# Performance work log

Measured on AMD Instinct MI355X. Metric: run time of the kernel, lower is better.

The kernel has to match this reference:

```python
import jax, jax.numpy as jnp
import numpy as np

MESSAGE_PASSES = 3
HID = 100        # hidden_node_features == message_size
EDGE_F = 4       # n_edge_features
OUT = 100        # readout output dim


def setup_inputs() -> dict:
    key = jax.random.key(0)
    ks = jax.random.split(key, 8)
    B, N = 32, 128
    nodes = jax.random.normal(ks[0], (B, N, HID), dtype=jnp.float32)
    edges = jax.random.uniform(ks[1], (B, N, N, EDGE_F), dtype=jnp.float32)
    s = 1.0 / np.sqrt(HID)
    Wv = jax.random.normal(ks[2], (HID, HID), dtype=jnp.float32) * s
    Ww = jax.random.normal(ks[3], (HID, HID), dtype=jnp.float32) * s
    We = jax.random.normal(ks[4], (EDGE_F, HID), dtype=jnp.float32) * (1.0 / np.sqrt(EDGE_F))
    Wu = jax.random.normal(ks[5], (2 * HID, HID), dtype=jnp.float32) * (1.0 / np.sqrt(2 * HID))
    Wr = jax.random.normal(ks[6], (2 * HID, OUT), dtype=jnp.float32) * (1.0 / np.sqrt(2 * HID))
    return {"nodes": nodes, "edges": edges, "Wv": Wv, "Ww": Ww, "We": We, "Wu": Wu, "Wr": Wr}


def reference(nodes, edges, Wv, Ww, We, Wu, Wr):
    # adjacency[b,v,w] = sum_e edges[b,v,w,e]; nonzero entries define the edge set
    adjacency = edges.sum(axis=-1)                       # [B,N,N]
    edge_mask = adjacency != 0                           # [B,N,N]
    node_mask = adjacency.sum(axis=-1) != 0              # [B,N]

    # edge feature projection is constant across message passes
    e_proj = jnp.einsum('bvwe,eh->bvwh', edges, We)      # [B,N,N,H]

    hidden = nodes                                       # hidden_node_features == node feat dim
    for _ in range(MESSAGE_PASSES):
        # message_terms for every (b, v, w) edge: relu(h_v Wv + h_w Ww + e_vw We)
        pre = (hidden @ Wv)[:, :, None, :] + (hidden @ Ww)[:, None, :, :] + e_proj
        mterms = jnp.where(edge_mask[..., None], jax.nn.relu(pre), 0.0)
        # (same_batch * same_node) matmul == segment-sum over neighbors w
        messages = mterms.sum(axis=2)                    # [B,N,H]
        # update only nodes that appear in the edge set (degree > 0)
        upd = jnp.tanh(jnp.concatenate([hidden, messages], axis=-1) @ Wu)
        hidden = jnp.where(node_mask[..., None], upd, hidden)

    # readout: masked sum-pool of per-node graph terms
    graph_terms = jax.nn.relu(jnp.concatenate([hidden, nodes], axis=-1) @ Wr)  # [B,N,OUT]
    output = jnp.where(node_mask[..., None], graph_terms, 0.0).sum(axis=1)     # [B,OUT]
    return output
```

## Files before the change

### kernel.cpp

```cpp
#include <hip/hip_runtime.h>
#include <math.h>

#define B_   32
#define N_   128
#define H_   100
#define ROWS (B_ * N_)
#define RH   (ROWS * H_)
#define OUTSZ (B_ * H_)

__global__ __launch_bounds__(256, 6) void k_proj0(const float* __restrict__ nodes,
                                                  const float* __restrict__ Ww,
                                                  float* __restrict__ hw,
                                                  float* __restrict__ out) {
    __shared__ float nod_s[2][H_];
    const int row0 = blockIdx.x * 2;
    const int t = threadIdx.x, r = t >> 7, j = t & 127;
    {
        const int gid = blockIdx.x * 256 + t;
        if (gid < OUTSZ) out[gid] = 0.f;
    }
    {
        const float4* ng = (const float4*)(nodes + (size_t)row0 * H_);
        if (t < 50) ((float4*)nod_s)[t] = ng[t];
    }
    __syncthreads();
    if (j >= H_) return;
    const float4* h4p = (const float4*)nod_s[r];
    float wa = 0.f;
#pragma unroll 5
    for (int k4 = 0; k4 < 25; ++k4) {
        const float4 h4 = h4p[k4];
        const int k = k4 * 4;
        wa = fmaf(h4.x, Ww[(k + 0) * H_ + j], wa);
        wa = fmaf(h4.y, Ww[(k + 1) * H_ + j], wa);
        wa = fmaf(h4.z, Ww[(k + 2) * H_ + j], wa);
        wa = fmaf(h4.w, Ww[(k + 3) * H_ + j], wa);
    }
    hw[(size_t)(row0 + r) * H_ + j] = wa;
}

template <int MODE, int INIT_HV>
__global__ __launch_bounds__(256, 6) void k_pass(const float* __restrict__ edges,
                                                 const float* __restrict__ We,
                                                 const float* __restrict__ Wu,
                                                 const float* __restrict__ Wv,
                                                 const float* __restrict__ Ww,
                                                 const float* __restrict__ Wr,
                                                 const float* __restrict__ nodes,
                                                 float* __restrict__ hv_io,
                                                 const float* __restrict__ hw_in,
                                                 float* __restrict__ hw_out,
                                                 const float* __restrict__ hid_in,
                                                 float* __restrict__ hidden,
                                                 float* __restrict__ out) {
    __shared__ float4 e_s[2][N_];
    __shared__ float  asum_part[4];
    __shared__ unsigned qmask_s[2][4];
    __shared__ float  hid_s[2][H_];
    __shared__ float  msg_s[2][H_];
    __shared__ float  hn_s[2][H_];
    __shared__ float  nod_s[2][H_];
    __shared__ float  red_s[2][H_];

    const int bx = blockIdx.x;
    const int cu = bx & 255, slot = bx >> 8;
    const int b = cu >> 3;
    const int vt = (cu & 7) + slot * 8;
    const int row0 = b * N_ + vt * 2;

    const int t = threadIdx.x, r = t >> 7, j = t & 127;
    const int wv = t >> 6, lane = t & 63;
    const int row = row0 + r;
    const bool act = (j < H_);

    {
        const float4* eg = (const float4*)(edges + (size_t)row0 * N_ * 4);
        const float4 e = eg[t];
        e_s[r][j] = e;
        float s = (e.x + e.y) + (e.z + e.w);
        const unsigned long long bal = __ballot(s != 0.f);
        if (lane == 0) {
            qmask_s[wv >> 1][(wv & 1) * 2]     = (unsigned)bal;
            qmask_s[wv >> 1][(wv & 1) * 2 + 1] = (unsigned)(bal >> 32);
        }
#pragma unroll
        for (int off = 32; off > 0; off >>= 1) s += __shfl_down(s, off);
        if (lane == 0) asum_part[wv] = s;
    }
    {
        const float4* hg = (const float4*)(hid_in + (size_t)row0 * H_);
        if (t < 50) ((float4*)hid_s)[t] = hg[t];
        if (MODE == 2) {
            const float4* ng = (const float4*)(nodes + (size_t)row0 * H_);
            if (t < 50) ((float4*)nod_s)[t] = ng[t];
        }
    }
    __syncthreads();

    const float nm = ((asum_part[2 * r] + asum_part[2 * r + 1]) != 0.f) ? 1.f : 0.f;

    if (act) {
        float hvv;
        if (INIT_HV) {
            const float4* h4p = (const float4*)hid_s[r];
            float va = 0.f;
#pragma unroll 5
            for (int k4 = 0; k4 < 25; ++k4) {
                const float4 h4 = h4p[k4];
                const int k = k4 * 4;
                va = fmaf(h4.x, Wv[(k + 0) * H_ + j], va);
                va = fmaf(h4.y, Wv[(k + 1) * H_ + j], va);
                va = fmaf(h4.z, Wv[(k + 2) * H_ + j], va);
                va = fmaf(h4.w, Wv[(k + 3) * H_ + j], va);
            }
            hvv = va;
        } else {
            hvv = hv_io[(size_t)row * H_ + j];
        }
        const float we0 = We[0 * H_ + j], we1 = We[1 * H_ + j];
        const float we2 = We[2 * H_ + j], we3 = We[3 * H_ + j];
        const float* hwp = hw_in + (size_t)b * N_ * H_ + j;
        float acc = 0.f;
        for (int c = 0; c < 4; ++c) {
            const unsigned mq =
                __builtin_amdgcn_readfirstlane(qmask_s[r][c]);
            const float4* ec = &e_s[r][c * 32];
            const float*  hc = hwp + (size_t)(c * 32) * H_;
#pragma unroll 8
            for (int w8 = 0; w8 < 32; ++w8) {
                const float4 e = ec[w8];
                const float  hww = hc[w8 * H_];
                const float  m = ((mq >> w8) & 1u) ? 1.f : 0.f;
                float p = hvv + hww;
                p = fmaf(e.x, we0, p);
                p = fmaf(e.y, we1, p);
                p = fmaf(e.z, we2, p);
                p = fmaf(e.w, we3, p);
                acc = fmaf(m, fmaxf(p, 0.f), acc);
            }
        }
        msg_s[r][j] = acc;
    }
    __syncthreads();

    if (act) {
        const float4* h4p = (const float4*)hid_s[r];
        const float4* m4p = (const float4*)msg_s[r];
        float u = 0.f;
#pragma unroll 5
        for (int k4 = 0; k4 < 25; ++k4) {
            const float4 h4 = h4p[k4];
            const int k = k4 * 4;
            u = fmaf(h4.x, Wu[(k + 0) * H_ + j], u);
            u = fmaf(h4.y, Wu[(k + 1) * H_ + j], u);
            u = fmaf(h4.z, Wu[(k + 2) * H_ + j], u);
            u = fmaf(h4.w, Wu[(k + 3) * H_ + j], u);
        }
#pragma unroll 5
        for (int k4 = 0; k4 < 25; ++k4) {
            const float4 m4 = m4p[k4];
            const int k = H_ + k4 * 4;
            u = fmaf(m4.x, Wu[(k + 0) * H_ + j], u);
            u = fmaf(m4.y, Wu[(k + 1) * H_ + j], u);
            u = fmaf(m4.z, Wu[(k + 2) * H_ + j], u);
            u = fmaf(m4.w, Wu[(k + 3) * H_ + j], u);
        }
        const float nh = (nm != 0.f) ? tanhf(u) : hid_s[r][j];
        hn_s[r][j] = nh;
        if (MODE == 1) hidden[(size_t)row * H_ + j] = nh;
    }
    __syncthreads();

    if (MODE == 1) {
        if (act) {
            const float4* h4p = (const float4*)hn_s[r];
            float va = 0.f, wa = 0.f;
#pragma unroll 5
            for (int k4 = 0; k4 < 25; ++k4) {
                const float4 h4 = h4p[k4];
                const int k = k4 * 4;
                va = fmaf(h4.x, Wv[(k + 0) * H_ + j], va);
                wa = fmaf(h4.x, Ww[(k + 0) * H_ + j], wa);
                va = fmaf(h4.y, Wv[(k + 1) * H_ + j], va);
                wa = fmaf(h4.y, Ww[(k + 1) * H_ + j], wa);
                va = fmaf(h4.z, Wv[(k + 2) * H_ + j], va);
                wa = fmaf(h4.z, Ww[(k + 2) * H_ + j], wa);
                va = fmaf(h4.w, Wv[(k + 3) * H_ + j], va);
                wa = fmaf(h4.w, Ww[(k + 3) * H_ + j], wa);
            }
            hv_io[(size_t)row * H_ + j] = va;
            hw_out[(size_t)row * H_ + j] = wa;
        }
    } else {
        if (act) {
            const float4* h4p = (const float4*)hn_s[r];
            const float4* n4p = (const float4*)nod_s[r];
            float u = 0.f;
#pragma unroll 5
            for (int k4 = 0; k4 < 25; ++k4) {
                const float4 h4 = h4p[k4];
                const int k = k4 * 4;
                u = fmaf(h4.x, Wr[(k + 0) * H_ + j], u);
                u = fmaf(h4.y, Wr[(k + 1) * H_ + j], u);
                u = fmaf(h4.z, Wr[(k + 2) * H_ + j], u);
                u = fmaf(h4.w, Wr[(k + 3) * H_ + j], u);
            }
#pragma unroll 5
            for (int k4 = 0; k4 < 25; ++k4) {
                const float4 n4 = n4p[k4];
                const int k = H_ + k4 * 4;
                u = fmaf(n4.x, Wr[(k + 0) * H_ + j], u);
                u = fmaf(n4.y, Wr[(k + 1) * H_ + j], u);
                u = fmaf(n4.z, Wr[(k + 2) * H_ + j], u);
                u = fmaf(n4.w, Wr[(k + 3) * H_ + j], u);
            }
            red_s[r][j] = nm * fmaxf(u, 0.f);
        }
        __syncthreads();
        if (t < H_) atomicAdd(out + b * H_ + t, red_s[0][t] + red_s[1][t]);
    }
}

extern "C" void kernel_launch(void* const* d_in, const int* in_sizes, int n_in,
                              void* d_out, int out_size, void* d_ws, size_t ws_size,
                              hipStream_t stream) {
    const float* nodes = (const float*)d_in[0];
    const float* edges = (const float*)d_in[1];
    const float* Wv    = (const float*)d_in[2];
    const float* Ww    = (const float*)d_in[3];
    const float* We    = (const float*)d_in[4];
    const float* Wu    = (const float*)d_in[5];
    const float* Wr    = (const float*)d_in[6];
    float* out = (float*)d_out;

    float* hidden = (float*)d_ws;
    float* hv     = hidden + RH;
    float* hwA    = hv + RH;
    float* hwB    = hwA + RH;

    k_proj0<<<ROWS / 2, 256, 0, stream>>>(nodes, Ww, hwA, out);

    k_pass<1, 1><<<ROWS / 2, 256, 0, stream>>>(edges, We, Wu, Wv, Ww, Wr, nodes,
                                               hv, hwA, hwB, nodes, hidden, out);
    k_pass<1, 0><<<ROWS / 2, 256, 0, stream>>>(edges, We, Wu, Wv, Ww, Wr, nodes,
                                               hv, hwB, hwA, hidden, hidden, out);
    k_pass<2, 0><<<ROWS / 2, 256, 0, stream>>>(edges, We, Wu, Wv, Ww, Wr, nodes,
                                               hv, hwA, hwB, hidden, hidden, out);
}
```

Before: 198.9 us.

## Process four rows per block with two rows per thread to reuse loads

```diff
diff --git a/kernel.cpp b/kernel.cpp
--- a/kernel.cpp
+++ b/kernel.cpp
@@ -53,171 +53,236 @@
                                                  const float* __restrict__ hid_in,
                                                  float* __restrict__ hidden,
                                                  float* __restrict__ out) {
-    __shared__ float4 e_s[2][N_];
-    __shared__ float  asum_part[4];
-    __shared__ unsigned qmask_s[2][4];
-    __shared__ float  hid_s[2][H_];
-    __shared__ float  msg_s[2][H_];
-    __shared__ float  hn_s[2][H_];
-    __shared__ float  nod_s[2][H_];
-    __shared__ float  red_s[2][H_];
+    __shared__ float4 e_s[4][N_];
+    __shared__ float  asum_s[4][2];
+    __shared__ unsigned qmask_s[4][4];
+    __shared__ float  hid_s[4][H_];
+    __shared__ float  msg_s[4][H_];
+    __shared__ float  hn_s[4][H_];
+    __shared__ float  nod_s[4][H_];
+    __shared__ float  red_s[4][H_];
 
     const int bx = blockIdx.x;
     const int cu = bx & 255, slot = bx >> 8;
     const int b = cu >> 3;
     const int vt = (cu & 7) + slot * 8;
-    const int row0 = b * N_ + vt * 2;
-
-    const int t = threadIdx.x, r = t >> 7, j = t & 127;
+    const int row0 = b * N_ + vt * 4;
+
+    const int t = threadIdx.x, rg = t >> 7, j = t & 127;
     const int wv = t >> 6, lane = t & 63;
-    const int row = row0 + r;
+    const int ra = rg * 2, rb = ra + 1;
+    const int rowA = row0 + ra, rowB = row0 + rb;
     const bool act = (j < H_);
 
     {
         const float4* eg = (const float4*)(edges + (size_t)row0 * N_ * 4);
-        const float4 e = eg[t];
-        e_s[r][j] = e;
-        float s = (e.x + e.y) + (e.z + e.w);
-        const unsigned long long bal = __ballot(s != 0.f);
-        if (lane == 0) {
-            qmask_s[wv >> 1][(wv & 1) * 2]     = (unsigned)bal;
-            qmask_s[wv >> 1][(wv & 1) * 2 + 1] = (unsigned)(bal >> 32);
-        }
+        float4* es = &e_s[0][0];
 #pragma unroll
-        for (int off = 32; off > 0; off >>= 1) s += __shfl_down(s, off);
-        if (lane == 0) asum_part[wv] = s;
+        for (int q = 0; q < 2; ++q) {
+            const int idx = q * 256 + t;
+            const float4 e = eg[idx];
+            es[idx] = e;
+            float s = (e.x + e.y) + (e.z + e.w);
+            const unsigned long long bal = __ballot(s != 0.f);
+            const int seg = q * 4 + wv;
+            const int rowq = seg >> 1, half = seg & 1;
+            if (lane == 0) {
+                qmask_s[rowq][half * 2]     = (unsigned)bal;
+                qmask_s[rowq][half * 2 + 1] = (unsigned)(bal >> 32);
+            }
+#pragma unroll
+            for (int off = 32; off > 0; off >>= 1) s += __shfl_down(s, off);
+            if (lane == 0) asum_s[rowq][half] = s;
+        }
     }
     {
         const float4* hg = (const float4*)(hid_in + (size_t)row0 * H_);
-        if (t < 50) ((float4*)hid_s)[t] = hg[t];
+        if (t < 100) ((float4*)hid_s)[t] = hg[t];
         if (MODE == 2) {
             const float4* ng = (const float4*)(nodes + (size_t)row0 * H_);
-            if (t < 50) ((float4*)nod_s)[t] = ng[t];
+            if (t < 100) ((float4*)nod_s)[t] = ng[t];
         }
     }
     __syncthreads();
 
-    const float nm = ((asum_part[2 * r] + asum_part[2 * r + 1]) != 0.f) ? 1.f : 0.f;
+    const float nmA = ((asum_s[ra][0] + asum_s[ra][1]) != 0.f) ? 1.f : 0.f;
+    const float nmB = ((asum_s[rb][0] + asum_s[rb][1]) != 0.f) ? 1.f : 0.f;
 
     if (act) {
-        float hvv;
+        float hvA, hvB;
         if (INIT_HV) {
-            const float4* h4p = (const float4*)hid_s[r];
-            float va = 0.f;
+            const float4* hA = (const float4*)hid_s[ra];
+            const float4* hB = (const float4*)hid_s[rb];
+            float vA = 0.f, vB = 0.f;
 #pragma unroll 5
             for (int k4 = 0; k4 < 25; ++k4) {
-                const float4 h4 = h4p[k4];
                 const int k = k4 * 4;
-                va = fmaf(h4.x, Wv[(k + 0) * H_ + j], va);
-                va = fmaf(h4.y, Wv[(k + 1) * H_ + j], va);
-                va = fmaf(h4.z, Wv[(k + 2) * H_ + j], va);
-                va = fmaf(h4.w, Wv[(k + 3) * H_ + j], va);
-            }
-            hvv = va;
+                const float w0 = Wv[(k + 0) * H_ + j];
+                const float w1 = Wv[(k + 1) * H_ + j];
+                const float w2 = Wv[(k + 2) * H_ + j];
+                const float w3 = Wv[(k + 3) * H_ + j];
+                const float4 a = hA[k4], c = hB[k4];
+                vA = fmaf(a.x, w0, vA); vB = fmaf(c.x, w0, vB);
+                vA = fmaf(a.y, w1, vA); vB = fmaf(c.y, w1, vB);
+                vA = fmaf(a.z, w2, vA); vB = fmaf(c.z, w2, vB);
+                vA = fmaf(a.w, w3, vA); vB = fmaf(c.w, w3, vB);
+            }
+            hvA = vA; hvB = vB;
         } else {
-            hvv = hv_io[(size_t)row * H_ + j];
+            hvA = hv_io[(size_t)rowA * H_ + j];
+            hvB = hv_io[(size_t)rowB * H_ + j];
         }
         const float we0 = We[0 * H_ + j], we1 = We[1 * H_ + j];
         const float we2 = We[2 * H_ + j], we3 = We[3 * H_ + j];
         const float* hwp = hw_in + (size_t)b * N_ * H_ + j;
-        float acc = 0.f;
+        float accA = 0.f, accB = 0.f;
         for (int c = 0; c < 4; ++c) {
-            const unsigned mq =
-                __builtin_amdgcn_readfirstlane(qmask_s[r][c]);
-            const float4* ec = &e_s[r][c * 32];
-            const float*  hc = hwp + (size_t)(c * 32) * H_;
+            const unsigned mqA =
+                __builtin_amdgcn_readfirstlane(qmask_s[ra][c]);
+            const unsigned mqB =
+                __builtin_amdgcn_readfirstlane(qmask_s[rb][c]);
+            const float4* ecA = &e_s[ra][c * 32];
+            const float4* ecB = &e_s[rb][c * 32];
+            const float*  hc  = hwp + (size_t)(c * 32) * H_;
 #pragma unroll 8
             for (int w8 = 0; w8 < 32; ++w8) {
-                const float4 e = ec[w8];
-                const float  hww = hc[w8 * H_];
-                const float  m = ((mq >> w8) & 1u) ? 1.f : 0.f;
-                float p = hvv + hww;
-                p = fmaf(e.x, we0, p);
-                p = fmaf(e.y, we1, p);
-                p = fmaf(e.z, we2, p);
-                p = fmaf(e.w, we3, p);
-                acc = fmaf(m, fmaxf(p, 0.f), acc);
-            }
-        }
-        msg_s[r][j] = acc;
+                const float hww = hc[w8 * H_];
+                const float4 eA = ecA[w8];
+                const float4 eB = ecB[w8];
+                float pA = hvA + hww;
+                pA = fmaf(eA.x, we0, pA);
+                pA = fmaf(eA.y, we1, pA);
+                pA = fmaf(eA.z, we2, pA);
+                pA = fmaf(eA.w, we3, pA);
+                const float mA = ((mqA >> w8) & 1u) ? 1.f : 0.f;
+                accA = fmaf(mA, fmaxf(pA, 0.f), accA);
+                float pB = hvB + hww;
+                pB = fmaf(eB.x, we0, pB);
+                pB = fmaf(eB.y, we1, pB);
+                pB = fmaf(eB.z, we2, pB);
+                pB = fmaf(eB.w, we3, pB);
+                const float mB = ((mqB >> w8) & 1u) ? 1.f : 0.f;
+                accB = fmaf(mB, fmaxf(pB, 0.f), accB);
+            }
+        }
+        msg_s[ra][j] = accA;
+        msg_s[rb][j] = accB;
     }
     __syncthreads();
 
+    float nhA, nhB;
     if (act) {
-        const float4* h4p = (const float4*)hid_s[r];
-        const float4* m4p = (const float4*)msg_s[r];
-        float u = 0.f;
+        const float4* hA = (const float4*)hid_s[ra];
+        const float4* hB = (const float4*)hid_s[rb];
+        const float4* mA4 = (const float4*)msg_s[ra];
+        const float4* mB4 = (const float4*)msg_s[rb];
+        float uA = 0.f, uB = 0.f;
 #pragma unroll 5
         for (int k4 = 0; k4 < 25; ++k4) {
-            const float4 h4 = h4p[k4];
             const int k = k4 * 4;
-            u = fmaf(h4.x, Wu[(k + 0) * H_ + j], u);
-            u = fmaf(h4.y, Wu[(k + 1) * H_ + j], u);
-            u = fmaf(h4.z, Wu[(k + 2) * H_ + j], u);
-            u = fmaf(h4.w, Wu[(k + 3) * H_ + j], u);
+            const float w0 = Wu[(k + 0) * H_ + j];
+            const float w1 = Wu[(k + 1) * H_ + j];
+            const float w2 = Wu[(k + 2) * H_ + j];
+            const float w3 = Wu[(k + 3) * H_ + j];
+            const float4 a = hA[k4], c = hB[k4];
+            uA = fmaf(a.x, w0, uA); uB = fmaf(c.x, w0, uB);
+            uA = fmaf(a.y, w1, uA); uB = fmaf(c.y, w1, uB);
+            uA = fmaf(a.z, w2, uA); uB = fmaf(c.z, w2, uB);
+            uA = fmaf(a.w, w3, uA); uB = fmaf(c.w, w3, uB);
         }
 #pragma unroll 5
         for (int k4 = 0; k4 < 25; ++k4) {
-            const float4 m4 = m4p[k4];
             const int k = H_ + k4 * 4;
-            u = fmaf(m4.x, Wu[(k + 0) * H_ + j], u);
-            u = fmaf(m4.y, Wu[(k + 1) * H_ + j], u);
-            u = fmaf(m4.z, Wu[(k + 2) * H_ + j], u);
-            u = fmaf(m4.w, Wu[(k + 3) * H_ + j], u);
-        }
-        const float nh = (nm != 0.f) ? tanhf(u) : hid_s[r][j];
-        hn_s[r][j] = nh;
-        if (MODE == 1) hidden[(size_t)row * H_ + j] = nh;
+            const float w0 = Wu[(k + 0) * H_ + j];
+            const float w1 = Wu[(k + 1) * H_ + j];
+            const float w2 = Wu[(k + 2) * H_ + j];
+            const float w3 = Wu[(k + 3) * H_ + j];
+            const float4 a = mA4[k4], c = mB4[k4];
+            uA = fmaf(a.x, w0, uA); uB = fmaf(c.x, w0, uB);
+            uA = fmaf(a.y, w1, uA); uB = fmaf(c.y, w1, uB);
+            uA = fmaf(a.z, w2, uA); uB = fmaf(c.z, w2, uB);
+            uA = fmaf(a.w, w3, uA); uB = fmaf(c.w, w3, uB);
+        }
+        nhA = (nmA != 0.f) ? tanhf(uA) : hid_s[ra][j];
+        nhB = (nmB != 0.f) ? tanhf(uB) : hid_s[rb][j];
+        hn_s[ra][j] = nhA;
+        hn_s[rb][j] = nhB;
+        if (MODE == 1) {
+            hidden[(size_t)rowA * H_ + j] = nhA;
+            hidden[(size_t)rowB * H_ + j] = nhB;
+        }
     }
     __syncthreads();
 
     if (MODE == 1) {
         if (act) {
-            const float4* h4p = (const float4*)hn_s[r];
-            float va = 0.f, wa = 0.f;
+            const float4* hA = (const float4*)hn_s[ra];
+            const float4* hB = (const float4*)hn_s[rb];
+            float vA = 0.f, wA = 0.f, vB = 0.f, wB = 0.f;
 #pragma unroll 5
             for (int k4 = 0; k4 < 25; ++k4) {
-                const float4 h4 = h4p[k4];
                 const int k = k4 * 4;
-                va = fmaf(h4.x, Wv[(k + 0) * H_ + j], va);
-                wa = fmaf(h4.x, Ww[(k + 0) * H_ + j], wa);
-                va = fmaf(h4.y, Wv[(k + 1) * H_ + j], va);
-                wa = fmaf(h4.y, Ww[(k + 1) * H_ + j], wa);
-                va = fmaf(h4.z, Wv[(k + 2) * H_ + j], va);
-                wa = fmaf(h4.z, Ww[(k + 2) * H_ + j], wa);
-                va = fmaf(h4.w, Wv[(k + 3) * H_ + j], va);
-                wa = fmaf(h4.w, Ww[(k + 3) * H_ + j], wa);
-            }
-            hv_io[(size_t)row * H_ + j] = va;
-            hw_out[(size_t)row * H_ + j] = wa;
+                const float v0 = Wv[(k + 0) * H_ + j], q0 = Ww[(k + 0) * H_ + j];
+                const float v1 = Wv[(k + 1) * H_ + j], q1 = Ww[(k + 1) * H_ + j];
+                const float v2 = Wv[(k + 2) * H_ + j], q2 = Ww[(k + 2) * H_ + j];
+                const float v3 = Wv[(k + 3) * H_ + j], q3 = Ww[(k + 3) * H_ + j];
+                const float4 a = hA[k4], c = hB[k4];
+                vA = fmaf(a.x, v0, vA); wA = fmaf(a.x, q0, wA);
+                vB = fmaf(c.x, v0, vB); wB = fmaf(c.x, q0, wB);
+                vA = fmaf(a.y, v1, vA); wA = fmaf(a.y, q1, wA);
+                vB = fmaf(c.y, v1, vB); wB = fmaf(c.y, q1, wB);
+                vA = fmaf(a.z, v2, vA); wA = fmaf(a.z, q2, wA);
+                vB = fmaf(c.z, v2, vB); wB = fmaf(c.z, q2, wB);
+                vA = fmaf(a.w, v3, vA); wA = fmaf(a.w, q3, wA);
+                vB = fmaf(c.w, v3, vB); wB = fmaf(c.w, q3, wB);
+            }
+            hv_io[(size_t)rowA * H_ + j] = vA;
+            hv_io[(size_t)rowB * H_ + j] = vB;
+            hw_out[(size_t)rowA * H_ + j] = wA;
+            hw_out[(size_t)rowB * H_ + j] = wB;
         }
     } else {
         if (act) {
-            const float4* h4p = (const float4*)hn_s[r];
-            const float4* n4p = (const float4*)nod_s[r];
-            float u = 0.f;
+            const float4* hA = (const float4*)hn_s[ra];
+            const float4* hB = (const float4*)hn_s[rb];
+            const float4* nA = (const float4*)nod_s[ra];
+            const float4* nB = (const float4*)nod_s[rb];
+            float uA = 0.f, uB = 0.f;
 #pragma unroll 5
             for (int k4 = 0; k4 < 25; ++k4) {
-                const float4 h4 = h4p[k4];
                 const int k = k4 * 4;
-                u = fmaf(h4.x, Wr[(k + 0) * H_ + j], u);
-                u = fmaf(h4.y, Wr[(k + 1) * H_ + j], u);
-                u = fmaf(h4.z, Wr[(k + 2) * H_ + j], u);
-                u = fmaf(h4.w, Wr[(k + 3) * H_ + j], u);
+                const float w0 = Wr[(k + 0) * H_ + j];
+                const float w1 = Wr[(k + 1) * H_ + j];
+                const float w2 = Wr[(k + 2) * H_ + j];
+                const float w3 = Wr[(k + 3) * H_ + j];
+                const float4 a = hA[k4], c = hB[k4];
+                uA = fmaf(a.x, w0, uA); uB = fmaf(c.x, w0, uB);
+                uA = fmaf(a.y, w1, uA); uB = fmaf(c.y, w1, uB);
+                uA = fmaf(a.z, w2, uA); uB = fmaf(c.z, w2, uB);
+                uA = fmaf(a.w, w3, uA); uB = fmaf(c.w, w3, uB);
             }
 #pragma unroll 5
             for (int k4 = 0; k4 < 25; ++k4) {
-                const float4 n4 = n4p[k4];
                 const int k = H_ + k4 * 4;
-                u = fmaf(n4.x, Wr[(k + 0) * H_ + j], u);
-                u = fmaf(n4.y, Wr[(k + 1) * H_ + j], u);
-                u = fmaf(n4.z, Wr[(k + 2) * H_ + j], u);
-                u = fmaf(n4.w, Wr[(k + 3) * H_ + j], u);
-            }
-            red_s[r][j] = nm * fmaxf(u, 0.f);
+                const float w0 = Wr[(k + 0) * H_ + j];
+                const float w1 = Wr[(k + 1) * H_ + j];
+                const float w2 = Wr[(k + 2) * H_ + j];
+                const float w3 = Wr[(k + 3) * H_ + j];
+                const float4 a = nA[k4], c = nB[k4];
+                uA = fmaf(a.x, w0, uA); uB = fmaf(c.x, w0, uB);
+                uA = fmaf(a.y, w1, uA); uB = fmaf(c.y, w1, uB);
+                uA = fmaf(a.z, w2, uA); uB = fmaf(c.z, w2, uB);
+                uA = fmaf(a.w, w3, uA); uB = fmaf(c.w, w3, uB);
+            }
+            red_s[ra][j] = nmA * fmaxf(uA, 0.f);
+            red_s[rb][j] = nmB * fmaxf(uB, 0.f);
         }
         __syncthreads();
-        if (t < H_) atomicAdd(out + b * H_ + t, red_s[0][t] + red_s[1][t]);
+        if (t < H_) {
+            const float ssum = (red_s[0][t] + red_s[1][t]) +
+                               (red_s[2][t] + red_s[3][t]);
+            atomicAdd(out + b * H_ + t, ssum);
+        }
     }
 }
 
@@ -240,10 +305,10 @@
 
     k_proj0<<<ROWS / 2, 256, 0, stream>>>(nodes, Ww, hwA, out);
 
-    k_pass<1, 1><<<ROWS / 2, 256, 0, stream>>>(edges, We, Wu, Wv, Ww, Wr, nodes,
+    k_pass<1, 1><<<ROWS / 4, 256, 0, stream>>>(edges, We, Wu, Wv, Ww, Wr, nodes,
                                                hv, hwA, hwB, nodes, hidden, out);
-    k_pass<1, 0><<<ROWS / 2, 256, 0, stream>>>(edges, We, Wu, Wv, Ww, Wr, nodes,
+    k_pass<1, 0><<<ROWS / 4, 256, 0, stream>>>(edges, We, Wu, Wv, Ww, Wr, nodes,
                                                hv, hwB, hwA, hidden, hidden, out);
-    k_pass<2, 0><<<ROWS / 2, 256, 0, stream>>>(edges, We, Wu, Wv, Ww, Wr, nodes,
+    k_pass<2, 0><<<ROWS / 4, 256, 0, stream>>>(edges, We, Wu, Wv, Ww, Wr, nodes,
                                                hv, hwA, hwB, hidden, hidden, out);
 }
```

Measured after the change: 226.9 us. +14.1%, slower.

## Split fused pass kernel into message and GEMM kernels with NaN-sentinel node mask

Applied to the files above, without the earlier changes.

```diff
diff --git a/kernel.cpp b/kernel.cpp
--- a/kernel.cpp
+++ b/kernel.cpp
@@ -39,28 +39,18 @@
     hw[(size_t)(row0 + r) * H_ + j] = wa;
 }
 
-template <int MODE, int INIT_HV>
-__global__ __launch_bounds__(256, 6) void k_pass(const float* __restrict__ edges,
-                                                 const float* __restrict__ We,
-                                                 const float* __restrict__ Wu,
-                                                 const float* __restrict__ Wv,
-                                                 const float* __restrict__ Ww,
-                                                 const float* __restrict__ Wr,
-                                                 const float* __restrict__ nodes,
-                                                 float* __restrict__ hv_io,
-                                                 const float* __restrict__ hw_in,
-                                                 float* __restrict__ hw_out,
-                                                 const float* __restrict__ hid_in,
-                                                 float* __restrict__ hidden,
-                                                 float* __restrict__ out) {
+template <int INIT_HV>
+__global__ __launch_bounds__(256, 8) void k_msg(const float* __restrict__ edges,
+                                                const float* __restrict__ We,
+                                                const float* __restrict__ Wv,
+                                                const float* __restrict__ hv_in,
+                                                const float* __restrict__ hw_in,
+                                                const float* __restrict__ hid_in,
+                                                float* __restrict__ msg) {
     __shared__ float4 e_s[2][N_];
     __shared__ float  asum_part[4];
     __shared__ unsigned qmask_s[2][4];
     __shared__ float  hid_s[2][H_];
-    __shared__ float  msg_s[2][H_];
-    __shared__ float  hn_s[2][H_];
-    __shared__ float  nod_s[2][H_];
-    __shared__ float  red_s[2][H_];
 
     const int bx = blockIdx.x;
     const int cu = bx & 255, slot = bx >> 8;
@@ -87,9 +77,91 @@
         for (int off = 32; off > 0; off >>= 1) s += __shfl_down(s, off);
         if (lane == 0) asum_part[wv] = s;
     }
-    {
+    if (INIT_HV) {
         const float4* hg = (const float4*)(hid_in + (size_t)row0 * H_);
         if (t < 50) ((float4*)hid_s)[t] = hg[t];
+    }
+    __syncthreads();
+
+    const float nm = ((asum_part[2 * r] + asum_part[2 * r + 1]) != 0.f) ? 1.f : 0.f;
+    if (!act) return;
+
+    float hvv;
+    if (INIT_HV) {
+        const float4* h4p = (const float4*)hid_s[r];
+        float va = 0.f;
+#pragma unroll 5
+        for (int k4 = 0; k4 < 25; ++k4) {
+            const float4 h4 = h4p[k4];
+            const int k = k4 * 4;
+            va = fmaf(h4.x, Wv[(k + 0) * H_ + j], va);
+            va = fmaf(h4.y, Wv[(k + 1) * H_ + j], va);
+            va = fmaf(h4.z, Wv[(k + 2) * H_ + j], va);
+            va = fmaf(h4.w, Wv[(k + 3) * H_ + j], va);
+        }
+        hvv = va;
+    } else {
+        hvv = hv_in[(size_t)row * H_ + j];
+    }
+    const float we0 = We[0 * H_ + j], we1 = We[1 * H_ + j];
+    const float we2 = We[2 * H_ + j], we3 = We[3 * H_ + j];
+    const float* hwp = hw_in + (size_t)b * N_ * H_ + j;
+    float acc = 0.f;
+    for (int c = 0; c < 4; ++c) {
+        const unsigned mq =
+            __builtin_amdgcn_readfirstlane(qmask_s[r][c]);
+        const float4* ec = &e_s[r][c * 32];
+        const float*  hc = hwp + (size_t)(c * 32) * H_;
+#pragma unroll 8
+        for (int w8 = 0; w8 < 32; ++w8) {
+            const float4 e = ec[w8];
+            const float  hww = hc[w8 * H_];
+            const float  m = ((mq >> w8) & 1u) ? 1.f : 0.f;
+            float p = hvv + hww;
+            p = fmaf(e.x, we0, p);
+            p = fmaf(e.y, we1, p);
+            p = fmaf(e.z, we2, p);
+            p = fmaf(e.w, we3, p);
+            acc = fmaf(m, fmaxf(p, 0.f), acc);
+        }
+    }
+    const float sent = __uint_as_float(0x7FC00000u);
+    msg[(size_t)row * H_ + j] = (j == 0 && nm == 0.f) ? sent : acc;
+}
+
+template <int MODE>
+__global__ __launch_bounds__(256, 8) void k_gemm(const float* __restrict__ Wu,
+                                                 const float* __restrict__ Wv,
+                                                 const float* __restrict__ Ww,
+                                                 const float* __restrict__ Wr,
+                                                 const float* __restrict__ nodes,
+                                                 const float* __restrict__ msg_in,
+                                                 const float* __restrict__ hid_in,
+                                                 float* __restrict__ hidden,
+                                                 float* __restrict__ hv_out,
+                                                 float* __restrict__ hw_out,
+                                                 float* __restrict__ out) {
+    __shared__ float hid_s[2][H_];
+    __shared__ float msg_s[2][H_];
+    __shared__ float hn_s[2][H_];
+    __shared__ float nod_s[2][H_];
+    __shared__ float red_s[2][H_];
+
+    const int bx = blockIdx.x;
+    const int cu = bx & 255, slot = bx >> 8;
+    const int b = cu >> 3;
+    const int vt = (cu & 7) + slot * 8;
+    const int row0 = b * N_ + vt * 2;
+
+    const int t = threadIdx.x, r = t >> 7, j = t & 127;
+    const int row = row0 + r;
+    const bool act = (j < H_);
+
+    {
+        const float4* hg = (const float4*)(hid_in + (size_t)row0 * H_);
+        if (t < 50) ((float4*)hid_s)[t] = hg[t];
+        const float4* mg = (const float4*)(msg_in + (size_t)row0 * H_);
+        if (t < 50) ((float4*)msg_s)[t] = mg[t];
         if (MODE == 2) {
             const float4* ng = (const float4*)(nodes + (size_t)row0 * H_);
             if (t < 50) ((float4*)nod_s)[t] = ng[t];
@@ -97,51 +169,8 @@
     }
     __syncthreads();
 
-    const float nm = ((asum_part[2 * r] + asum_part[2 * r + 1]) != 0.f) ? 1.f : 0.f;
-
-    if (act) {
-        float hvv;
-        if (INIT_HV) {
-            const float4* h4p = (const float4*)hid_s[r];
-            float va = 0.f;
-#pragma unroll 5
-            for (int k4 = 0; k4 < 25; ++k4) {
-                const float4 h4 = h4p[k4];
-                const int k = k4 * 4;
-                va = fmaf(h4.x, Wv[(k + 0) * H_ + j], va);
-                va = fmaf(h4.y, Wv[(k + 1) * H_ + j], va);
-                va = fmaf(h4.z, Wv[(k + 2) * H_ + j], va);
-                va = fmaf(h4.w, Wv[(k + 3) * H_ + j], va);
-            }
-            hvv = va;
-        } else {
-            hvv = hv_io[(size_t)row * H_ + j];
-        }
-        const float we0 = We[0 * H_ + j], we1 = We[1 * H_ + j];
-        const float we2 = We[2 * H_ + j], we3 = We[3 * H_ + j];
-        const float* hwp = hw_in + (size_t)b * N_ * H_ + j;
-        float acc = 0.f;
-        for (int c = 0; c < 4; ++c) {
-            const unsigned mq =
-                __builtin_amdgcn_readfirstlane(qmask_s[r][c]);
-            const float4* ec = &e_s[r][c * 32];
-            const float*  hc = hwp + (size_t)(c * 32) * H_;
-#pragma unroll 8
-            for (int w8 = 0; w8 < 32; ++w8) {
-                const float4 e = ec[w8];
-                const float  hww = hc[w8 * H_];
-                const float  m = ((mq >> w8) & 1u) ? 1.f : 0.f;
-                float p = hvv + hww;
-                p = fmaf(e.x, we0, p);
-                p = fmaf(e.y, we1, p);
-                p = fmaf(e.z, we2, p);
-                p = fmaf(e.w, we3, p);
-                acc = fmaf(m, fmaxf(p, 0.f), acc);
-            }
-        }
-        msg_s[r][j] = acc;
-    }
-    __syncthreads();
+    const unsigned mb0 = __float_as_uint(msg_s[r][0]);
+    const bool nmb = ((mb0 & 0x7fffffffu) <= 0x7f800000u);
 
     if (act) {
         const float4* h4p = (const float4*)hid_s[r];
@@ -165,7 +194,7 @@
             u = fmaf(m4.z, Wu[(k + 2) * H_ + j], u);
             u = fmaf(m4.w, Wu[(k + 3) * H_ + j], u);
         }
-        const float nh = (nm != 0.f) ? tanhf(u) : hid_s[r][j];
+        const float nh = nmb ? tanhf(u) : hid_s[r][j];
         hn_s[r][j] = nh;
         if (MODE == 1) hidden[(size_t)row * H_ + j] = nh;
     }
@@ -188,7 +217,7 @@
                 va = fmaf(h4.w, Wv[(k + 3) * H_ + j], va);
                 wa = fmaf(h4.w, Ww[(k + 3) * H_ + j], wa);
             }
-            hv_io[(size_t)row * H_ + j] = va;
+            hv_out[(size_t)row * H_ + j] = va;
             hw_out[(size_t)row * H_ + j] = wa;
         }
     } else {
@@ -214,7 +243,7 @@
                 u = fmaf(n4.z, Wr[(k + 2) * H_ + j], u);
                 u = fmaf(n4.w, Wr[(k + 3) * H_ + j], u);
             }
-            red_s[r][j] = nm * fmaxf(u, 0.f);
+            red_s[r][j] = nmb ? fmaxf(u, 0.f) : 0.f;
         }
         __syncthreads();
         if (t < H_) atomicAdd(out + b * H_ + t, red_s[0][t] + red_s[1][t]);
@@ -240,10 +269,13 @@
 
     k_proj0<<<ROWS / 2, 256, 0, stream>>>(nodes, Ww, hwA, out);
 
-    k_pass<1, 1><<<ROWS / 2, 256, 0, stream>>>(edges, We, Wu, Wv, Ww, Wr, nodes,
-                                               hv, hwA, hwB, nodes, hidden, out);
-    k_pass<1, 0><<<ROWS / 2, 256, 0, stream>>>(edges, We, Wu, Wv, Ww, Wr, nodes,
-                                               hv, hwB, hwA, hidden, hidden, out);
-    k_pass<2, 0><<<ROWS / 2, 256, 0, stream>>>(edges, We, Wu, Wv, Ww, Wr, nodes,
-                                               hv, hwA, hwB, hidden, hidden, out);
-}
+    k_msg<1><<<ROWS / 2, 256, 0, stream>>>(edges, We, Wv, hv, hwA, nodes, hwB);
+    k_gemm<1><<<ROWS / 2, 256, 0, stream>>>(Wu, Wv, Ww, Wr, nodes, hwB, nodes,
+                                            hidden, hv, hwB, out);
+    k_msg<0><<<ROWS / 2, 256, 0, stream>>>(edges, We, Wv, hv, hwB, hidden, hwA);
+    k_gemm<1><<<ROWS / 2, 256, 0, stream>>>(Wu, Wv, Ww, Wr, nodes, hwA, hidden,
+                                            hidden, hv, hwA, out);
+    k_msg<0><<<ROWS / 2, 256, 0, stream>>>(edges, We, Wv, hv, hwA, hidden, hwB);
+    k_gemm<2><<<ROWS / 2, 256, 0, stream>>>(Wu, Wv, Ww, Wr, nodes, hwB, hidden,
+                                            hidden, hv, hwB, out);
+}
```

New measurement: 241.6 us. 1.21x slower.
